# Performance work log

Hardware: AMD Instinct MI355X
Metric: run time of the kernel (lower is better)

The kernel has to match this reference:

```python
import jax, jax.numpy as jnp
import numpy as np

N, F_IN, F_OUT, HEADS = 4096, 128, 64, 4


def setup_inputs() -> dict:
    key = jax.random.key(0)
    k1, k2, k3, k4, k5 = jax.random.split(key, 5)
    X = jax.random.normal(k1, (N, F_IN), dtype=jnp.float32)
    A = jax.random.randint(k2, (N, N), 0, 2, dtype=jnp.int32)
    # zero the diagonal: the torch loop always prepends the self node, so the
    # adjacency must not also contain it (would duplicate the self term).
    A = A * (1 - jnp.eye(N, dtype=jnp.int32))
    # per-head Linear(F_IN, F_OUT) weights/bias and Linear(2*F_OUT, 1, bias=False)
    W = jax.random.normal(k3, (HEADS, F_OUT, F_IN), dtype=jnp.float32) / np.sqrt(F_IN)
    b = jax.random.normal(k4, (HEADS, F_OUT), dtype=jnp.float32) * 0.02
    att = jax.random.normal(k5, (HEADS, 2 * F_OUT), dtype=jnp.float32) / np.sqrt(2 * F_OUT)
    return {"X": X, "A": A, "W": W, "b": b, "att": att}


def reference(X, A, W, b, att):
    # H[h, n, o] = line_h(X)
    H = jnp.einsum('nf,hof->hno', X, W) + b[:, None, :]
    f_out = W.shape[1]
    a_src, a_dst = att[:, :f_out], att[:, f_out:]
    # score e_ij = leaky_relu(a_src.H_i + a_dst.H_j)
    s = jnp.einsum('hno,ho->hn', H, a_src)  # query-side term (xi_bar expanded)
    d = jnp.einsum('hno,ho->hn', H, a_dst)  # neighbor-side term
    e = jax.nn.leaky_relu(s[:, :, None] + d[:, None, :])  # [H, N, N]
    # neighbor set = {self} U {j : A_ij != 0}
    mask = (A > 0) | jnp.eye(A.shape[0], dtype=bool)
    e = jnp.where(mask[None], e, -jnp.inf)
    alpha = jax.nn.softmax(e, axis=-1)  # segment softmax per node row
    # weighted sum per head, then mean over heads (sum / head in the original)
    out = jnp.einsum('hnm,hmo->no', alpha, H) / W.shape[0]
    return out  # [N, F_OUT]
```

## Files before the change

### kernel.cpp

```cpp
#include <hip/hip_runtime.h>
#include <hip/hip_bf16.h>


#define NN 4096
#define FIN 128
#define FOUT 64
#define NH 4

typedef __attribute__((ext_vector_type(8))) short bf16x8;
typedef __attribute__((ext_vector_type(4))) float f32x4;
typedef __attribute__((ext_vector_type(4))) unsigned int u32x4;

__device__ __forceinline__ unsigned short f32_bf16(float f) {
    unsigned u = __builtin_bit_cast(unsigned, f);
    u += 0x7fffu + ((u >> 16) & 1u);
    return (unsigned short)(u >> 16);
}

__global__ __launch_bounds__(256) void pack_bits(
    const int* __restrict__ A, unsigned long long* __restrict__ Abits)
{
    const int row  = blockIdx.x;
    const int lane = threadIdx.x & 63;
    const int wv   = threadIdx.x >> 6;
    const int* arow = A + (size_t)row * NN;
    #pragma unroll 4
    for (int c = 0; c < 16; ++c) {
        const int col = c * 256 + wv * 64 + lane;
        unsigned long long m = __ballot(__builtin_nontemporal_load(&arow[col]) > 0);
        if (lane == 0) Abits[(size_t)row * 64 + c * 4 + wv] = m;
    }
}

__global__ __launch_bounds__(256) void gat_prep(
    const float* __restrict__ X, const float* __restrict__ W,
    const float* __restrict__ b, const float* __restrict__ att,
    unsigned short* __restrict__ HbfT, float* __restrict__ Hrow,
    float* __restrict__ s_out, float* __restrict__ d_out,
    float* __restrict__ es_g, float* __restrict__ es2_g,
    float* __restrict__ ed_g, float* __restrict__ ed2_g)
{
    const int rb = blockIdx.x;
    const int h  = blockIdx.y;
    const int n0 = rb * 32;
    const int t  = threadIdx.x;

    __shared__ float Xl[32][132];
    __shared__ float Wt[128][68];

    for (int g = t; g < 32 * 32; g += 256) {
        int row = g >> 5, c4 = g & 31;
        float4 v = *(const float4*)&X[(size_t)(n0 + row) * FIN + c4 * 4];
        *(float4*)&Xl[row][c4 * 4] = v;
    }
    for (int g = t; g < 64 * 32; g += 256) {
        int o = g >> 5, c4 = g & 31;
        float4 v = *(const float4*)&W[((size_t)h * FOUT + o) * FIN + c4 * 4];
        Wt[c4 * 4 + 0][o] = v.x; Wt[c4 * 4 + 1][o] = v.y;
        Wt[c4 * 4 + 2][o] = v.z; Wt[c4 * 4 + 3][o] = v.w;
    }
    __syncthreads();

    const int rg = t >> 4;
    const int og = t & 15;
    float acc[2][4] = {};

    #pragma unroll 4
    for (int f4 = 0; f4 < 32; ++f4) {
        float xv[2][4], wv[4][4];
        #pragma unroll
        for (int i = 0; i < 2; ++i) {
            float4 tmp = *(const float4*)&Xl[rg * 2 + i][f4 * 4];
            xv[i][0] = tmp.x; xv[i][1] = tmp.y; xv[i][2] = tmp.z; xv[i][3] = tmp.w;
        }
        #pragma unroll
        for (int k = 0; k < 4; ++k) {
            float4 tmp = *(const float4*)&Wt[f4 * 4 + k][og * 4];
            wv[k][0] = tmp.x; wv[k][1] = tmp.y; wv[k][2] = tmp.z; wv[k][3] = tmp.w;
        }
        #pragma unroll
        for (int i = 0; i < 2; ++i)
            #pragma unroll
            for (int k = 0; k < 4; ++k)
                #pragma unroll
                for (int jj = 0; jj < 4; ++jj)
                    acc[i][jj] = fmaf(xv[i][k], wv[k][jj], acc[i][jj]);
    }

    float bb[4], as_[4], ad_[4];
    #pragma unroll
    for (int jj = 0; jj < 4; ++jj) {
        bb[jj]  = b[h * FOUT + og * 4 + jj];
        as_[jj] = att[h * 2 * FOUT + og * 4 + jj];
        ad_[jj] = att[h * 2 * FOUT + FOUT + og * 4 + jj];
    }
    #pragma unroll
    for (int i = 0; i < 2; ++i)
        #pragma unroll
        for (int jj = 0; jj < 4; ++jj)
            acc[i][jj] += bb[jj];

    float sp[2] = {0.f, 0.f}, dp[2] = {0.f, 0.f};
    #pragma unroll
    for (int i = 0; i < 2; ++i)
        #pragma unroll
        for (int jj = 0; jj < 4; ++jj) {
            sp[i] = fmaf(acc[i][jj], as_[jj], sp[i]);
            dp[i] = fmaf(acc[i][jj], ad_[jj], dp[i]);
        }
    #pragma unroll
    for (int off = 1; off < 16; off <<= 1) {
        #pragma unroll
        for (int i = 0; i < 2; ++i) {
            sp[i] += __shfl_xor(sp[i], off);
            dp[i] += __shfl_xor(dp[i], off);
        }
    }
    if (og == 0) {
        #pragma unroll
        for (int i = 0; i < 2; ++i) {
            int nn = n0 + rg * 2 + i;
            s_out[h * NN + nn]  = sp[i];
            d_out[h * NN + nn]  = dp[i];
            es_g [h * NN + nn]  = __expf(sp[i]);
            es2_g[h * NN + nn]  = __expf(0.01f * sp[i]);
            ed_g [h * NN + nn]  = __expf(dp[i]);
            ed2_g[h * NN + nn]  = __expf(0.01f * dp[i]);
        }
    }

    #pragma unroll
    for (int i = 0; i < 2; ++i) {
        float4 v = make_float4(acc[i][0], acc[i][1], acc[i][2], acc[i][3]);
        *(float4*)&Hrow[((size_t)h * NN + n0 + rg * 2 + i) * FOUT + og * 4] = v;
    }
    #pragma unroll
    for (int jj = 0; jj < 4; ++jj) {
        int o = og * 4 + jj;
        ushort2 p;
        p.x = f32_bf16(acc[0][jj]);
        p.y = f32_bf16(acc[1][jj]);
        *(ushort2*)&HbfT[((size_t)h * FOUT + o) * NN + n0 + rg * 2] = p;
    }
}

struct SMem {
    union {
        struct {
            __align__(16) unsigned short H[2][64][128];
            unsigned bits[2][32 * 5];
        } st;
        struct {
            float red[6][16][68];
            float redl[6][16];
        } fin;
    };
};

__global__ __launch_bounds__(512, 4) void gat_main(
    const unsigned* __restrict__ Abits, const unsigned short* __restrict__ HbfT,
    const float* __restrict__ s_g, const float* __restrict__ d_g,
    const float* __restrict__ es_g, const float* __restrict__ es2_g,
    const float* __restrict__ ed_g, const float* __restrict__ ed2_g,
    const float* __restrict__ Hrow, float* __restrict__ outH)
{
    const int id   = blockIdx.x;
    const int h    = id & 3;
    const int tile = id >> 2;
    const int n0   = tile * 32;
    const int tid  = threadIdx.x;
    const int w    = tid >> 6;
    const int lane = tid & 63;
    const int r    = lane & 15;
    const int q    = lane >> 4;
    const int qs   = q * 8;
    const int rg   = w & 1;
    const int kg   = w >> 1;

    __shared__ SMem sm;

    const int nrow = n0 + rg * 16 + r;
    const float es  = es_g [h * NN + nrow];
    const float es2 = es2_g[h * NN + nrow];

    const int mb       = (kg * 4 + q) ^ r;
    const int bits_idx = (rg * 16 + r) * 5 + kg;

    const int so = tid >> 4;
    const int sc = tid & 15;
    const unsigned short* srcA = HbfT + ((size_t)(h * FOUT) + so)      * NN + sc * 8;
    const unsigned short* srcB = HbfT + ((size_t)(h * FOUT) + so + 32) * NN + sc * 8;
    const int offA = so * 128        + (sc ^ (so & 15)) * 8;
    const int offB = (so + 32) * 128 + (sc ^ (so & 15)) * 8;
    const int brow = tid >> 2, bwd = tid & 3;
    const unsigned* srcBits = Abits + (size_t)(n0 + brow) * 128 + bwd;

    const float* edh  = ed_g  + h * NN + kg * 32 + qs;
    const float* ed2h = ed2_g + h * NN + kg * 32 + qs;

    bf16x8 ones;
    #pragma unroll
    for (int i = 0; i < 8; ++i) ones[i] = (short)0x3F80;

    f32x4 acc0 = {0,0,0,0}, acc1 = {0,0,0,0}, acc2 = {0,0,0,0},
          acc3 = {0,0,0,0}, accl = {0,0,0,0};

    bf16x8 stA, stB;
    unsigned stBits = 0;

    stA = *(const bf16x8*)&srcA[0];
    stB = *(const bf16x8*)&srcB[0];
    {
        unsigned short* hw = &sm.st.H[0][0][0];
        *(bf16x8*)(hw + offA) = stA;
        *(bf16x8*)(hw + offB) = stB;
        if (tid < 128) sm.st.bits[0][brow * 5 + bwd] = srcBits[0];
    }
    __syncthreads();

    for (int ch = 0; ch < 32; ++ch) {
        const int buf = ch & 1;
        const unsigned short* hb = buf ? &sm.st.H[1][0][0] : &sm.st.H[0][0][0];
        const unsigned*       bl = buf ? sm.st.bits[1]     : sm.st.bits[0];

        if (ch < 31) {
            stA = *(const bf16x8*)&srcA[(ch + 1) * 128];
            stB = *(const bf16x8*)&srcB[(ch + 1) * 128];
            if (tid < 128) stBits = srcBits[(ch + 1) * 4];
        }

        const unsigned bits8 = bl[bits_idx] >> qs;
        const int cb = ch * 128;
        const float4 e0 = *(const float4*)&edh [cb];
        const float4 e1 = *(const float4*)&edh [cb + 4];
        const float4 g0 = *(const float4*)&ed2h[cb];
        const float4 g1 = *(const float4*)&ed2h[cb + 4];
        const float edv [8] = {e0.x, e0.y, e0.z, e0.w, e1.x, e1.y, e1.z, e1.w};
        const float ed2v[8] = {g0.x, g0.y, g0.z, g0.w, g1.x, g1.y, g1.z, g1.w};

        u32x4 afu;
        #pragma unroll
        for (int p = 0; p < 4; ++p) {
            const int j0 = 2 * p, j1 = 2 * p + 1;
            float wa = (bits8 & (1u << j0))
                     ? fmaxf(es * edv[j0], es2 * ed2v[j0]) : 0.0f;
            float wb = (bits8 & (1u << j1))
                     ? fmaxf(es * edv[j1], es2 * ed2v[j1]) : 0.0f;
            __hip_bfloat162 pk = __float22bfloat162_rn(make_float2(wa, wb));
            unsigned u;
            __builtin_memcpy(&u, &pk, sizeof(u));
            afu[p] = u;
        }
        const bf16x8 af = __builtin_bit_cast(bf16x8, afu);

        const bf16x8 b0 = *(const bf16x8*)&hb[(r     ) * 128 + mb * 8];
        const bf16x8 b1 = *(const bf16x8*)&hb[(r + 16) * 128 + mb * 8];
        const bf16x8 b2 = *(const bf16x8*)&hb[(r + 32) * 128 + mb * 8];
        const bf16x8 b3 = *(const bf16x8*)&hb[(r + 48) * 128 + mb * 8];

        acc0 = __builtin_amdgcn_mfma_f32_16x16x32_bf16(af, b0,   acc0, 0, 0, 0);
        acc1 = __builtin_amdgcn_mfma_f32_16x16x32_bf16(af, b1,   acc1, 0, 0, 0);
        acc2 = __builtin_amdgcn_mfma_f32_16x16x32_bf16(af, b2,   acc2, 0, 0, 0);
        acc3 = __builtin_amdgcn_mfma_f32_16x16x32_bf16(af, b3,   acc3, 0, 0, 0);
        accl = __builtin_amdgcn_mfma_f32_16x16x32_bf16(af, ones, accl, 0, 0, 0);

        if (ch < 31) {
            unsigned short* hw = buf ? &sm.st.H[0][0][0] : &sm.st.H[1][0][0];
            *(bf16x8*)(hw + offA) = stA;
            *(bf16x8*)(hw + offB) = stB;
            if (tid < 128) (buf ? sm.st.bits[0] : sm.st.bits[1])[brow * 5 + bwd] = stBits;
        }
        __syncthreads();
    }

    if (kg > 0) {
        const int widx = (kg - 1) * 2 + rg;
        #pragma unroll
        for (int reg = 0; reg < 4; ++reg) {
            const int rr = q * 4 + reg;
            sm.fin.red[widx][rr][ 0 + r] = acc0[reg];
            sm.fin.red[widx][rr][16 + r] = acc1[reg];
            sm.fin.red[widx][rr][32 + r] = acc2[reg];
            sm.fin.red[widx][rr][48 + r] = acc3[reg];
        }
        if (r == 0) {
            #pragma unroll
            for (int reg = 0; reg < 4; ++reg)
                sm.fin.redl[widx][q * 4 + reg] = accl[reg];
        }
    }
    __syncthreads();
    if (kg == 0) {
        #pragma unroll
        for (int kk = 0; kk < 3; ++kk) {
            const int widx = kk * 2 + rg;
            #pragma unroll
            for (int reg = 0; reg < 4; ++reg) {
                const int rr = q * 4 + reg;
                acc0[reg] += sm.fin.red[widx][rr][ 0 + r];
                acc1[reg] += sm.fin.red[widx][rr][16 + r];
                acc2[reg] += sm.fin.red[widx][rr][32 + r];
                acc3[reg] += sm.fin.red[widx][rr][48 + r];
                accl[reg] += sm.fin.redl[widx][rr];
            }
        }
        #pragma unroll
        for (int reg = 0; reg < 4; ++reg) {
            const int rr  = q * 4 + reg;
            const int nn2 = n0 + rg * 16 + rr;
            const float tt = s_g[h * NN + nn2] + d_g[h * NN + nn2];
            const float wd = __expf(fmaxf(tt, 0.01f * tt));
            const float inv = 0.25f / (accl[reg] + wd);
            const float* hr = &Hrow[((size_t)h * NN + nn2) * FOUT];
            float*       ob = &outH[((size_t)h * NN + nn2) * FOUT];
            ob[ 0 + r] = (acc0[reg] + wd * hr[ 0 + r]) * inv;
            ob[16 + r] = (acc1[reg] + wd * hr[16 + r]) * inv;
            ob[32 + r] = (acc2[reg] + wd * hr[32 + r]) * inv;
            ob[48 + r] = (acc3[reg] + wd * hr[48 + r]) * inv;
        }
    }
}

__global__ __launch_bounds__(256) void gat_fin(
    const float* __restrict__ outH, float* __restrict__ out)
{
    const int i = blockIdx.x * 256 + threadIdx.x;
    const f32x4* p = (const f32x4*)outH;
    f32x4 v0 = __builtin_nontemporal_load(p + i);
    f32x4 v1 = __builtin_nontemporal_load(p + i +  65536);
    f32x4 v2 = __builtin_nontemporal_load(p + i + 131072);
    f32x4 v3 = __builtin_nontemporal_load(p + i + 196608);
    f32x4 s = (v0 + v1) + (v2 + v3);
    *((f32x4*)out + i) = s;
}

extern "C" void kernel_launch(void* const* d_in, const int* in_sizes, int n_in,
                              void* d_out, int out_size, void* d_ws, size_t ws_size,
                              hipStream_t stream) {
    const float* X   = (const float*)d_in[0];
    const int*   A   = (const int*)  d_in[1];
    const float* W   = (const float*)d_in[2];
    const float* b   = (const float*)d_in[3];
    const float* att = (const float*)d_in[4];
    float* out = (float*)d_out;

    char* ws = (char*)d_ws;
    unsigned short* HbfT = (unsigned short*)ws;
    size_t off = (size_t)NH * FOUT * NN * 2;
    float* s_buf   = (float*)(ws + off);  off += (size_t)NH * NN * 4;
    float* d_buf   = (float*)(ws + off);  off += (size_t)NH * NN * 4;
    float* es_buf  = (float*)(ws + off);  off += (size_t)NH * NN * 4;
    float* es2_buf = (float*)(ws + off);  off += (size_t)NH * NN * 4;
    float* ed_buf  = (float*)(ws + off);  off += (size_t)NH * NN * 4;
    float* ed2_buf = (float*)(ws + off);  off += (size_t)NH * NN * 4;
    unsigned long long* Abits = (unsigned long long*)(ws + off);
    off += (size_t)NN * 64 * 8;
    float* Hrow   = (float*)(ws + off);
    off += (size_t)NH * NN * FOUT * 4;
    float* outH   = (float*)(ws + off);
    off += (size_t)NH * NN * FOUT * 4;

    pack_bits<<<NN, 256, 0, stream>>>(A, Abits);
    gat_prep<<<dim3(128, 4), 256, 0, stream>>>(X, W, b, att, HbfT, Hrow,
                                               s_buf, d_buf,
                                               es_buf, es2_buf, ed_buf, ed2_buf);
    gat_main<<<512, 512, 0, stream>>>((const unsigned*)Abits, HbfT,
                                      s_buf, d_buf,
                                      es_buf, es2_buf, ed_buf, ed2_buf,
                                      Hrow, outH);
    gat_fin<<<256, 256, 0, stream>>>(outH, out);
}
```

Measured before the change: 167.7 us.

## Stage H, mask bits and ed terms via direct global-to-LDS triple buffering

Replaces the register-staged double buffer with `global_load_lds` async copies into a three-deep LDS ring. Each wave loads pre-swizzled H rows straight into shared memory, and three waves also stage the adjacency bits and the ed/ed2 vectors. Explicit `vmcnt` waits plus a single barrier per chunk replace the register round trip and the per-lane global ed loads. The aim is to remove VGPR staging and LDS write instructions and to hide load latency two chunks ahead. In exchange, LDS use rises to about 48KB per block, which may cut occupancy below the requested 4 blocks per CU.

```diff
diff --git a/kernel.cpp b/kernel.cpp
--- a/kernel.cpp
+++ b/kernel.cpp
@@ -15,6 +15,12 @@
     unsigned u = __builtin_bit_cast(unsigned, f);
     u += 0x7fffu + ((u >> 16) & 1u);
     return (unsigned short)(u >> 16);
+}
+
+__device__ __forceinline__ void gload16(const void* g, void* l) {
+    __builtin_amdgcn_global_load_lds(
+        (const __attribute__((address_space(1))) unsigned*)g,
+        (__attribute__((address_space(3))) unsigned*)l, 16, 0, 0);
 }
 
 __global__ __launch_bounds__(256) void pack_bits(
@@ -146,15 +152,15 @@
 
 struct SMem {
     union {
-        struct {
-            __align__(16) unsigned short H[2][64][128];
-            unsigned bits[2][32 * 5];
-        } st;
+        __align__(16) unsigned short H[3][64][128];
         struct {
             float red[6][16][68];
             float redl[6][16];
         } fin;
     };
+    unsigned bits[3][32][4];
+    float ed [3][128];
+    float ed2[3][128];
 };
 
 __global__ __launch_bounds__(512, 4) void gat_main(
@@ -183,20 +189,18 @@
     const float es  = es_g [h * NN + nrow];
     const float es2 = es2_g[h * NN + nrow];
 
-    const int mb       = (kg * 4 + q) ^ r;
-    const int bits_idx = (rg * 16 + r) * 5 + kg;
-
-    const int so = tid >> 4;
-    const int sc = tid & 15;
-    const unsigned short* srcA = HbfT + ((size_t)(h * FOUT) + so)      * NN + sc * 8;
-    const unsigned short* srcB = HbfT + ((size_t)(h * FOUT) + so + 32) * NN + sc * 8;
-    const int offA = so * 128        + (sc ^ (so & 15)) * 8;
-    const int offB = (so + 32) * 128 + (sc ^ (so & 15)) * 8;
-    const int brow = tid >> 2, bwd = tid & 3;
-    const unsigned* srcBits = Abits + (size_t)(n0 + brow) * 128 + bwd;
-
-    const float* edh  = ed_g  + h * NN + kg * 32 + qs;
-    const float* ed2h = ed2_g + h * NN + kg * 32 + qs;
+    const int sblk = ((kg * 4 + q) ^ r) & 15;
+
+    const int rowA = 8 * w + (lane >> 4);
+    const int rowB = rowA + 4;
+    const int blkL = lane & 15;
+    const unsigned short* gH0 =
+        HbfT + ((size_t)(h * FOUT) + rowA) * NN + (size_t)(blkL ^ (rowA & 15)) * 8;
+    const unsigned short* gH1 =
+        HbfT + ((size_t)(h * FOUT) + rowB) * NN + (size_t)(blkL ^ (rowB & 15)) * 8;
+    const unsigned* gBits = Abits + (size_t)(n0 + lane) * 128;
+    const float*    gEd   = ed_g  + (size_t)h * NN + lane * 4;
+    const float*    gEd2  = ed2_g + (size_t)h * NN + lane * 4;
 
     bf16x8 ones;
     #pragma unroll
@@ -205,39 +209,23 @@
     f32x4 acc0 = {0,0,0,0}, acc1 = {0,0,0,0}, acc2 = {0,0,0,0},
           acc3 = {0,0,0,0}, accl = {0,0,0,0};
 
-    bf16x8 stA, stB;
-    unsigned stBits = 0;
-
-    stA = *(const bf16x8*)&srcA[0];
-    stB = *(const bf16x8*)&srcB[0];
-    {
-        unsigned short* hw = &sm.st.H[0][0][0];
-        *(bf16x8*)(hw + offA) = stA;
-        *(bf16x8*)(hw + offB) = stB;
-        if (tid < 128) sm.st.bits[0][brow * 5 + bwd] = srcBits[0];
-    }
-    __syncthreads();
-
-    for (int ch = 0; ch < 32; ++ch) {
-        const int buf = ch & 1;
-        const unsigned short* hb = buf ? &sm.st.H[1][0][0] : &sm.st.H[0][0][0];
-        const unsigned*       bl = buf ? sm.st.bits[1]     : sm.st.bits[0];
-
-        if (ch < 31) {
-            stA = *(const bf16x8*)&srcA[(ch + 1) * 128];
-            stB = *(const bf16x8*)&srcB[(ch + 1) * 128];
-            if (tid < 128) stBits = srcBits[(ch + 1) * 4];
-        }
-
-        const unsigned bits8 = bl[bits_idx] >> qs;
-        const int cb = ch * 128;
-        const float4 e0 = *(const float4*)&edh [cb];
-        const float4 e1 = *(const float4*)&edh [cb + 4];
-        const float4 g0 = *(const float4*)&ed2h[cb];
-        const float4 g1 = *(const float4*)&ed2h[cb + 4];
+    auto STAGE = [&](int chn, int bt) {
+        const size_t coff = (size_t)chn * 128;
+        gload16(gH0 + coff, &sm.H[bt][8 * w][0]);
+        gload16(gH1 + coff, &sm.H[bt][8 * w + 4][0]);
+        if      (w == 3) { if (lane < 32) gload16(gBits + (size_t)chn * 4, &sm.bits[bt][0][0]); }
+        else if (w == 4) { if (lane < 32) gload16(gEd   + coff,            &sm.ed [bt][0]); }
+        else if (w == 5) { if (lane < 32) gload16(gEd2  + coff,            &sm.ed2[bt][0]); }
+    };
+
+    auto COMPUTE = [&](int bc) {
+        const unsigned bits8 = sm.bits[bc][rg * 16 + r][kg] >> qs;
+        const float4 e0 = *(const float4*)&sm.ed [bc][kg * 32 + qs];
+        const float4 e1 = *(const float4*)&sm.ed [bc][kg * 32 + qs + 4];
+        const float4 g0 = *(const float4*)&sm.ed2[bc][kg * 32 + qs];
+        const float4 g1 = *(const float4*)&sm.ed2[bc][kg * 32 + qs + 4];
         const float edv [8] = {e0.x, e0.y, e0.z, e0.w, e1.x, e1.y, e1.z, e1.w};
         const float ed2v[8] = {g0.x, g0.y, g0.z, g0.w, g1.x, g1.y, g1.z, g1.w};
-
         u32x4 afu;
         #pragma unroll
         for (int p = 0; p < 4; ++p) {
@@ -253,25 +241,38 @@
         }
         const bf16x8 af = __builtin_bit_cast(bf16x8, afu);
 
-        const bf16x8 b0 = *(const bf16x8*)&hb[(r     ) * 128 + mb * 8];
-        const bf16x8 b1 = *(const bf16x8*)&hb[(r + 16) * 128 + mb * 8];
-        const bf16x8 b2 = *(const bf16x8*)&hb[(r + 32) * 128 + mb * 8];
-        const bf16x8 b3 = *(const bf16x8*)&hb[(r + 48) * 128 + mb * 8];
+        const bf16x8 b0 = *(const bf16x8*)&sm.H[bc][r     ][sblk * 8];
+        const bf16x8 b1 = *(const bf16x8*)&sm.H[bc][r + 16][sblk * 8];
+        const bf16x8 b2 = *(const bf16x8*)&sm.H[bc][r + 32][sblk * 8];
+        const bf16x8 b3 = *(const bf16x8*)&sm.H[bc][r + 48][sblk * 8];
 
         acc0 = __builtin_amdgcn_mfma_f32_16x16x32_bf16(af, b0,   acc0, 0, 0, 0);
         acc1 = __builtin_amdgcn_mfma_f32_16x16x32_bf16(af, b1,   acc1, 0, 0, 0);
         acc2 = __builtin_amdgcn_mfma_f32_16x16x32_bf16(af, b2,   acc2, 0, 0, 0);
         acc3 = __builtin_amdgcn_mfma_f32_16x16x32_bf16(af, b3,   acc3, 0, 0, 0);
         accl = __builtin_amdgcn_mfma_f32_16x16x32_bf16(af, ones, accl, 0, 0, 0);
-
-        if (ch < 31) {
-            unsigned short* hw = buf ? &sm.st.H[0][0][0] : &sm.st.H[1][0][0];
-            *(bf16x8*)(hw + offA) = stA;
-            *(bf16x8*)(hw + offB) = stB;
-            if (tid < 128) (buf ? sm.st.bits[0] : sm.st.bits[1])[brow * 5 + bwd] = stBits;
-        }
-        __syncthreads();
-    }
+    };
+
+    STAGE(0, 0);
+    STAGE(1, 1);
+
+    int bc = 0;
+    for (int ch = 0; ch < 31; ++ch) {
+        if (w >= 3 && w <= 5) asm volatile("s_waitcnt vmcnt(3)" ::: "memory");
+        else                  asm volatile("s_waitcnt vmcnt(2)" ::: "memory");
+        __builtin_amdgcn_s_barrier();
+        if (ch + 2 < 32) {
+            int bt = bc + 2; if (bt >= 3) bt -= 3;
+            STAGE(ch + 2, bt);
+        }
+        COMPUTE(bc);
+        bc = (bc == 2) ? 0 : bc + 1;
+    }
+    asm volatile("s_waitcnt vmcnt(0)" ::: "memory");
+    __builtin_amdgcn_s_barrier();
+    COMPUTE(bc);
+
+    __syncthreads();
 
     if (kg > 0) {
         const int widx = (kg - 1) * 2 + rg;
```

Result: faster. 161.8 us (-3.5%).
